# Kernel tuning notes

Measured on AMD Instinct MI355X. Metric: run time of the kernel, lower is better.

## Reference

```python
import jax, jax.numpy as jnp
import numpy as np

B, T_IN, T_OUT, D, M, N = 4, 10, 5, 5, 96, 96
H1 = 64      # hidden dim of deep ConvLSTM layers
ATTN = 32    # attention bottleneck channels
SEL = 0      # selected_dim


def _conv(x, w, b):
    # SAME conv, NCHW / OIHW
    p = (w.shape[-1] - 1) // 2
    y = jax.lax.conv_general_dilated(x, w, (1, 1), [(p, p), (p, p)],
                                     dimension_numbers=('NCHW', 'OIHW', 'NCHW'))
    return y + b[None, :, None, None]


def _cell(xt, h, c, w, b):
    # standard ConvLSTM cell (no peephole): conv over concat(x, h) -> i,f,o,g
    z = _conv(jnp.concatenate([xt, h], axis=1), w, b)
    i, f, o, g = jnp.split(z, 4, axis=1)
    c = jax.nn.sigmoid(f) * c + jax.nn.sigmoid(i) * jnp.tanh(g)
    h = jax.nn.sigmoid(o) * jnp.tanh(c)
    return h, c


def setup_inputs() -> dict:
    key = jax.random.key(0)
    ks = jax.random.split(key, 12)
    w = lambda k, s: jax.random.normal(k, s, jnp.float32) * 0.05
    z = lambda n: jnp.zeros((n,), jnp.float32)
    return {
        'x': jax.random.normal(ks[0], (B, T_IN, D, M, N), jnp.float32),
        # encoder ConvLSTM cells: hidden dims [1, H1, H1]
        'enc_w0': w(ks[1], (4 * 1, D + 1, 3, 3)), 'enc_b0': z(4 * 1),
        'enc_w1': w(ks[2], (4 * H1, 1 + H1, 3, 3)), 'enc_b1': z(4 * H1),
        'enc_w2': w(ks[3], (4 * H1, H1 + H1, 3, 3)), 'enc_b2': z(4 * H1),
        # decoder ConvLSTM cells: hidden dims [H1, H1, 1]
        'dec_w0': w(ks[4], (4 * H1, 1 + H1, 3, 3)), 'dec_b0': z(4 * H1),
        'dec_w1': w(ks[5], (4 * H1, H1 + H1, 3, 3)), 'dec_b1': z(4 * H1),
        'dec_w2': w(ks[6], (4 * 1, H1 + 1, 3, 3)), 'dec_b2': z(4 * 1),
        # input attention (DA-RNN style with convs): e_k = v(tanh(Wi*x_k + Wh*[h;c]))
        'attn_wi': w(ks[7], (ATTN, T_IN, 3, 3)), 'attn_bi': z(ATTN),
        'attn_wh': w(ks[8], (ATTN, 2, 3, 3)), 'attn_bh': z(ATTN),
        'attn_wv': w(ks[9], (1, ATTN, 3, 3)), 'attn_bv': z(1),
        # temporal_cnn: Conv2d(1 + window_in, 1, kernel_size=1) + ReLU
        'tcnn_w': w(ks[10], (1, T_IN + 1, 1, 1)), 'tcnn_b': z(1),
    }


def reference(x, enc_w0, enc_b0, enc_w1, enc_b1, enc_w2, enc_b2,
              dec_w0, dec_b0, dec_w1, dec_b1, dec_w2, dec_b2,
              attn_wi, attn_bi, attn_wh, attn_bh, attn_wv, attn_bv,
              tcnn_w, tcnn_b):
    b = x.shape[0]

    def attn_reweight(xs, h, c):
        # xs: (b, t, d, m, n); hidden term shared across the d channels
        hid_e = _conv(jnp.concatenate([h, c], axis=1), attn_wh, attn_bh)
        def per_k(xk):  # (b, t, m, n): time-as-channels
            e = jnp.tanh(_conv(xk, attn_wi, attn_bi) + hid_e)
            return _conv(e, attn_wv, attn_bv)[:, 0]  # (b, m, n)
        alpha = jax.vmap(per_k, in_axes=2, out_axes=1)(xs)  # (b, d, m, n)
        ea = jnp.exp(alpha)
        return xs * (ea / jnp.max(ea))[:, None]  # global-max normalization

    def run_layer(xs, h, c, w, bb):
        def step(carry, xt):
            hh, cc = _cell(xt, carry[0], carry[1], w, bb)
            return (hh, cc), hh
        (h, c), hs = jax.lax.scan(step, (h, c), jnp.swapaxes(xs, 0, 1))
        return jnp.swapaxes(hs, 0, 1), (h, c)

    # ---------- encoder ----------
    h0 = jnp.zeros((b, 1, M, N), x.dtype); c0 = jnp.zeros_like(h0)
    def enc0_step(carry, t):
        xs, h, c = carry
        xs = attn_reweight(xs, h, c)  # re-weight whole sequence each step
        xt = jax.lax.dynamic_index_in_dim(xs, t, axis=1, keepdims=False)
        h, c = _cell(xt, h, c, enc_w0, enc_b0)
        return (xs, h, c), h
    (_, h0, c0), hs0 = jax.lax.scan(enc0_step, (x, h0, c0), jnp.arange(T_IN))
    out0 = jnp.swapaxes(hs0, 0, 1)  # (b, T_IN, 1, m, n)

    h1 = jnp.zeros((b, H1, M, N), x.dtype); c1 = jnp.zeros_like(h1)
    out1, (h1, c1) = run_layer(out0, h1, c1, enc_w1, enc_b1)
    h2 = jnp.zeros((b, H1, M, N), x.dtype); c2 = jnp.zeros_like(h2)
    out2, (h2, c2) = run_layer(out1, h2, c2, enc_w2, enc_b2)

    # ---------- decoder (encoder states reversed) ----------
    dec_in = jnp.zeros((b, T_OUT, 1, M, N), x.dtype)
    d0, _ = run_layer(dec_in, h2, c2, dec_w0, dec_b0)
    d1, _ = run_layer(d0, h1, c1, dec_w1, dec_b1)

    y_prev = x[:, :, SEL]  # (b, T_IN, m, n): selected variable, time-as-channels
    def dec2_step(carry, xt):
        h, c, yp = carry
        h, c = _cell(xt, h, c, dec_w2, dec_b2)          # (b, 1, m, n)
        ycat = jnp.concatenate([yp, h], axis=1)         # (b, T_IN+1, m, n)
        h = jax.nn.relu(_conv(ycat, tcnn_w, tcnn_b))    # temporal 1x1 CNN readout
        return (h, c, ycat[:, 1:]), h
    _, hs = jax.lax.scan(dec2_step, (h0, c0, y_prev), jnp.swapaxes(d1, 0, 1))
    return jnp.swapaxes(hs, 0, 1)  # (b, T_OUT, 1, m, n)
```

## Files before the change

### kernel.cpp

```cpp
#include <hip/hip_runtime.h>


#define PIX  9216
#define NB   4
#define TIN  10
#define TOUT 5
#define ND   5
#define HID  64

typedef __attribute__((ext_vector_type(8))) short bf16x8;
typedef __attribute__((ext_vector_type(4))) float f32x4;

__device__ __forceinline__ float sigmf_(float x) { return 1.0f / (1.0f + __expf(-x)); }
__device__ __forceinline__ float tanhf_(float x) { return 1.0f - 2.0f / (__expf(2.0f * x) + 1.0f); }
__device__ __forceinline__ unsigned short f2bf(float f) {
    unsigned u = __float_as_uint(f);
    unsigned r = u + 0x7FFFu + ((u >> 16) & 1u);
    return (unsigned short)(r >> 16);
}
__device__ __forceinline__ float bf2f(unsigned short u) {
    return __uint_as_float(((unsigned)u) << 16);
}
__device__ __forceinline__ unsigned fmap_(float f) {
    unsigned u = __float_as_uint(f);
    return (u & 0x80000000u) ? ~u : (u | 0x80000000u);
}
__device__ __forceinline__ float funmap_(unsigned v) {
    return __uint_as_float((v & 0x80000000u) ? (v ^ 0x80000000u) : ~v);
}
__device__ __forceinline__ void gload_lds16(const void* g, void* l) {
    __builtin_amdgcn_global_load_lds(
        (const __attribute__((address_space(1))) void*)g,
        (__attribute__((address_space(3))) void*)l, 16, 0, 0);
}

template <int NCH, bool XCONV>
__device__ __forceinline__ void
cell64_body(char* smem, int bid,
            const unsigned short* __restrict__ inP,
            const unsigned short* __restrict__ wP,
            const float* __restrict__ bias,
            const float* cprev, float* cout,
            const float* __restrict__ zeropg,
            unsigned short* __restrict__ d1, int d1_coff, int d1_ncg,
            unsigned short* __restrict__ d2, int d2_coff, int d2_ncg,
            const float* __restrict__ xim, const unsigned short* __restrict__ wxP)
{
    const int lane = threadIdx.x;
    const int wv   = threadIdx.y;
    const int tid  = wv * 64 + lane;
    const int rid = (bid & 7) * 48 + (bid >> 3);
    const int y = rid % 96, b = rid / 96;
    const int l15 = lane & 15, l4 = lane >> 4;
    const int NCG = NCH * 4;

    const int scg  = tid & 3;
    const int spr0 = tid >> 2;

    auto stage = [&](char* buf, int cc) {
#pragma unroll
        for (int i = 0; i < 5; ++i) {
            int pr = spr0 + i * 64;
            int r = pr / 98;
            int p = pr - r * 98;
            int gy = y - 1 + r, gx = p - 1;
            const void* g = (const void*)zeropg;
            if (pr < 294 && (unsigned)gy < 96u && (unsigned)gx < 96u) {
                int cg = scg ^ ((p >> 1) & 3);
                g = (const void*)(inP + (((size_t)(b * NCG + cc * 4 + cg) * 9216
                                          + gy * 96 + gx) << 3));
            }
            gload_lds16(g, buf + i * 4096 + wv * 1024);
        }
    };

    f32x4 acc[4][6] = {};
    bf16x8 af[3][4];

#pragma unroll
    for (int t0 = 0; t0 < 2; ++t0)
#pragma unroll
        for (int g = 0; g < 4; ++g)
            af[t0][g] = *(const bf16x8*)(wP
                + ((size_t)(t0 * NCH + 0) * 256 + g * 64 + wv * 16 + l15) * 32 + l4 * 8);

    stage(smem, 0);
    __syncthreads();
#pragma unroll
    for (int cc = 0; cc < NCH; ++cc) {
        if (cc + 1 < NCH) stage(smem + ((cc + 1) & 1) * 20480, cc + 1);
        const char* buf = smem + (cc & 1) * 20480;
#pragma unroll
        for (int tap = 0; tap < 9; ++tap) {
            const int T = cc * 9 + tap;
            const int Tp = T + 2;
            if (Tp < NCH * 9) {
                const int cc2 = Tp / 9, tap2 = Tp % 9;
#pragma unroll
                for (int g = 0; g < 4; ++g)
                    af[Tp % 3][g] = *(const bf16x8*)(wP
                        + ((size_t)(tap2 * NCH + cc2) * 256 + g * 64 + wv * 16 + l15) * 32 + l4 * 8);
            }
            const int ky = tap / 3, kx = tap % 3;
            bf16x8 bk[6];
#pragma unroll
            for (int k = 0; k < 6; ++k) {
                int p = k * 16 + kx + l15;
                int slot = l4 ^ ((p >> 1) & 3);
                bk[k] = *(const bf16x8*)(buf + (ky * 98 + p) * 64 + slot * 16);
            }
            __builtin_amdgcn_s_setprio(1);
#pragma unroll
            for (int g = 0; g < 4; ++g)
#pragma unroll
                for (int k = 0; k < 6; ++k)
                    acc[g][k] = __builtin_amdgcn_mfma_f32_16x16x32_bf16(
                        af[T % 3][g], bk[k], acc[g][k], 0, 0, 0);
            __builtin_amdgcn_s_setprio(0);
        }
        if (cc + 1 < NCH) __syncthreads();
    }

    if (XCONV) {
        bf16x8 afx[4];
#pragma unroll
        for (int g = 0; g < 4; ++g)
            afx[g] = *(const bf16x8*)(wxP
                + ((size_t)(g * 64 + wv * 16 + l15)) * 32 + l4 * 8);
        const float* xb = xim + b * PIX;
#pragma unroll
        for (int k = 0; k < 6; ++k) {
            int p = k * 16 + l15;
            bf16x8 bx = { 0, 0, 0, 0, 0, 0, 0, 0 };
#pragma unroll
            for (int j = 0; j < 8; ++j) {
                int tap = l4 * 8 + j;
                if (tap < 9) {
                    int gy = y + tap / 3 - 1, gx = p + tap % 3 - 1;
                    if ((unsigned)gy < 96u && (unsigned)gx < 96u)
                        bx[j] = (short)f2bf(xb[gy * 96 + gx]);
                }
            }
#pragma unroll
            for (int g = 0; g < 4; ++g)
                acc[g][k] = __builtin_amdgcn_mfma_f32_16x16x32_bf16(
                    afx[g], bx, acc[g][k], 0, 0, 0);
        }
    }

#pragma unroll
    for (int r = 0; r < 4; ++r) {
        int hc = wv * 16 + l4 * 4 + r;
        float bi = bias[hc], bff = bias[64 + hc];
        float bo = bias[128 + hc], bg = bias[192 + hc];
#pragma unroll
        for (int k = 0; k < 6; ++k) {
            int px = k * 16 + l15;
            int gpix = y * 96 + px;
            float ii = sigmf_(acc[0][k][r] + bi);
            float ff = sigmf_(acc[1][k][r] + bff);
            float oo = sigmf_(acc[2][k][r] + bo);
            float gg = tanhf_(acc[3][k][r] + bg);
            int cidx = (b * HID + hc) * 9216 + gpix;
            float cn = ff * cprev[cidx] + ii * gg;
            cout[cidx] = cn;
            unsigned short hb = f2bf(oo * tanhf_(cn));
            int ch1 = d1_coff + hc;
            d1[((size_t)(b * d1_ncg + (ch1 >> 3)) * 9216 + gpix) * 8 + (ch1 & 7)] = hb;
            if (d2) {
                int ch2 = d2_coff + hc;
                d2[((size_t)(b * d2_ncg + (ch2 >> 3)) * 9216 + gpix) * 8 + (ch2 & 7)] = hb;
            }
        }
    }
}

__device__ __forceinline__ void
attnE_body(char* smem, int aid,
           const unsigned short* __restrict__ xsp, const unsigned short* __restrict__ wiP,
           const float* __restrict__ h0, const float* __restrict__ c0,
           const float* __restrict__ wh, const float* __restrict__ bh,
           const float* __restrict__ bi, unsigned short* __restrict__ eP)
{
    float* heS = (float*)smem;
    const int lane = threadIdx.x, wvid = threadIdx.y;
    const int tile = aid % 36, k = (aid / 36) % 5, bb = aid / 180;
    const int l15 = lane & 15, l4 = lane >> 4;
    const int tid = wvid * 64 + lane;

    {
        int p = tile * 256 + tid;
        int y = p / 96, x = p - y * 96;
        float hv9[9], cv9[9];
        const float* hp = h0 + bb * PIX;
        const float* cp = c0 + bb * PIX;
#pragma unroll
        for (int t9 = 0; t9 < 9; ++t9) {
            int gy = y + t9 / 3 - 1, gx = x + t9 % 3 - 1;
            bool ok = (unsigned)gy < 96u && (unsigned)gx < 96u;
            hv9[t9] = ok ? hp[gy * 96 + gx] : 0.0f;
            cv9[t9] = ok ? cp[gy * 96 + gx] : 0.0f;
        }
#pragma unroll
        for (int ch = 0; ch < 32; ++ch) {
            float a = bi[ch] + bh[ch];
#pragma unroll
            for (int t9 = 0; t9 < 9; ++t9) {
                a = fmaf(wh[(ch * 2 + 0) * 9 + t9], hv9[t9], a);
                a = fmaf(wh[(ch * 2 + 1) * 9 + t9], cv9[t9], a);
            }
            heS[tid * 33 + ch] = a;
        }
    }

    bf16x8 af[5][2];
#pragma unroll
    for (int j = 0; j < 5; ++j)
#pragma unroll
        for (int m = 0; m < 2; ++m)
            af[j][m] = *(const bf16x8*)(wiP + ((size_t)(j * 32 + m * 16 + l15)) * 32 + l4 * 8);

    const unsigned short* xb = xsp + (size_t)(bb * ND + k) * PIX * 16;
    const int p0 = tile * 256 + wvid * 64;

    f32x4 acc[4][2] = {};
#pragma unroll
    for (int nf = 0; nf < 4; ++nf) {
        int p = p0 + nf * 16 + l15;
        int y = p / 96, x = p - y * 96;
#pragma unroll
        for (int j = 0; j < 5; ++j) {
            int tp = 2 * j + (l4 >> 1);
            bf16x8 bk = { 0, 0, 0, 0, 0, 0, 0, 0 };
            if (tp < 9) {
                int gy = y + tp / 3 - 1, gx = x + tp % 3 - 1;
                if ((unsigned)gy < 96u && (unsigned)gx < 96u)
                    bk = *(const bf16x8*)(xb + ((size_t)(gy * 96 + gx)) * 16 + (l4 & 1) * 8);
            }
            acc[nf][0] = __builtin_amdgcn_mfma_f32_16x16x32_bf16(af[j][0], bk, acc[nf][0], 0, 0, 0);
            acc[nf][1] = __builtin_amdgcn_mfma_f32_16x16x32_bf16(af[j][1], bk, acc[nf][1], 0, 0, 0);
        }
    }

    __syncthreads();

#pragma unroll
    for (int nf = 0; nf < 4; ++nf) {
        int p = p0 + nf * 16 + l15;
        int pl = wvid * 64 + nf * 16 + l15;
        const float* hrow = &heS[pl * 33];
#pragma unroll
        for (int m = 0; m < 2; ++m) {
            ushort4 o;
            o.x = f2bf(tanhf_(acc[nf][m][0] + hrow[m * 16 + l4 * 4 + 0]));
            o.y = f2bf(tanhf_(acc[nf][m][1] + hrow[m * 16 + l4 * 4 + 1]));
            o.z = f2bf(tanhf_(acc[nf][m][2] + hrow[m * 16 + l4 * 4 + 2]));
            o.w = f2bf(tanhf_(acc[nf][m][3] + hrow[m * 16 + l4 * 4 + 3]));
            *(ushort4*)(eP + ((size_t)(bb * ND + k) * PIX + p) * 32 + m * 16 + l4 * 4) = o;
        }
    }
}

__device__ __forceinline__ void
alpha_body(char* smem, int aid,
           const unsigned short* __restrict__ eP, const float* __restrict__ wvv,
           const float* __restrict__ bv, float* __restrict__ alpha,
           unsigned* __restrict__ msl)
{
    const int tid = threadIdx.y * 64 + threadIdx.x;
    const int tile = aid % 36, k = (aid / 36) % 5, bb = aid / 180;
    int p = tile * 256 + tid;
    int y = p / 96, x = p - y * 96;
    const unsigned short* eb = eP + (size_t)(bb * ND + k) * PIX * 32;
    float acc = bv[0];
#pragma unroll
    for (int ky = 0; ky < 3; ++ky) {
        int gy = y + ky - 1;
        if ((unsigned)gy >= 96u) continue;
#pragma unroll
        for (int kx = 0; kx < 3; ++kx) {
            int gx = x + kx - 1;
            if ((unsigned)gx >= 96u) continue;
            int tap = ky * 3 + kx;
            const unsigned short* ee = eb + ((size_t)(gy * 96 + gx)) * 32;
#pragma unroll
            for (int cg = 0; cg < 4; ++cg) {
                bf16x8 ev = *(const bf16x8*)(ee + cg * 8);
#pragma unroll
                for (int jj = 0; jj < 8; ++jj)
                    acc = fmaf(wvv[(cg * 8 + jj) * 9 + tap], bf2f((unsigned short)ev[jj]), acc);
            }
        }
    }
    alpha[(size_t)(bb * ND + k) * PIX + p] = acc;

    float* s = (float*)smem;
    s[tid] = acc;
    __syncthreads();
    for (int st = 128; st > 0; st >>= 1) {
        if (tid < st) s[tid] = fmaxf(s[tid], s[tid + st]);
        __syncthreads();
    }
    if (tid == 0) atomicMax(msl, fmap_(s[0]));
}

__device__ __forceinline__ void
dec2_body(int did,
          const unsigned short* __restrict__ inP, int ncg, int cgbase,
          const float* __restrict__ hprev, const float* cprev,
          const unsigned short* __restrict__ wm, const float* __restrict__ w2,
          const float* __restrict__ bias,
          const float* __restrict__ tw, const float* __restrict__ tb,
          const float* __restrict__ yprev,
          float* __restrict__ ynext, float* __restrict__ hcarry,
          float* __restrict__ outp, float* cout)
{
    const int wv = threadIdx.y, lane = threadIdx.x;
    const int l15 = lane & 15, l4 = lane >> 4;
    const int bx = did % 144, b = did / 144;
    const int p0 = (bx * 4 + wv) * 16;
    const int y = p0 / 96, xbase = p0 - y * 96;
    const int x = xbase + l15;

    f32x4 acc = {0.f, 0.f, 0.f, 0.f};
#pragma unroll
    for (int ky = 0; ky < 3; ++ky) {
        int gy = y + ky - 1;
        bool oky = (unsigned)gy < 96u;
#pragma unroll
        for (int kx = 0; kx < 3; ++kx) {
            const int tap = ky * 3 + kx;
            int gx = x + kx - 1;
            bool ok = oky && ((unsigned)gx < 96u);
#pragma unroll
            for (int cc = 0; cc < 2; ++cc) {
                bf16x8 a = *(const bf16x8*)(wm + ((size_t)(tap * 2 + cc) * 16 + l15) * 32 + l4 * 8);
                bf16x8 bk = { 0, 0, 0, 0, 0, 0, 0, 0 };
                if (ok)
                    bk = *(const bf16x8*)(inP + ((size_t)(b * ncg + cgbase + cc * 4 + l4) * 9216
                                                 + gy * 96 + gx) * 8);
                acc = __builtin_amdgcn_mfma_f32_16x16x32_bf16(a, bk, acc, 0, 0, 0);
            }
        }
    }

    if (l4 == 0) {
        int px = p0 + l15;
        float aI = acc[0] + bias[0];
        float aF = acc[1] + bias[1];
        float aO = acc[2] + bias[2];
        float aG = acc[3] + bias[3];
        const float* hp = hprev + b * PIX;
#pragma unroll
        for (int ky = 0; ky < 3; ++ky) {
            int gy = y + ky - 1;
            if ((unsigned)gy >= 96u) continue;
#pragma unroll
            for (int kx = 0; kx < 3; ++kx) {
                int gx = x + kx - 1;
                if ((unsigned)gx >= 96u) continue;
                int tap = ky * 3 + kx;
                float hv = hp[gy * 96 + gx];
                aI = fmaf(w2[(0 * 65 + 64) * 9 + tap], hv, aI);
                aF = fmaf(w2[(1 * 65 + 64) * 9 + tap], hv, aF);
                aO = fmaf(w2[(2 * 65 + 64) * 9 + tap], hv, aO);
                aG = fmaf(w2[(3 * 65 + 64) * 9 + tap], hv, aG);
            }
        }
        int idx = b * PIX + px;
        float cn = sigmf_(aF) * cprev[idx] + sigmf_(aI) * tanhf_(aG);
        cout[idx] = cn;
        float h = sigmf_(aO) * tanhf_(cn);

        float a2 = tb[0];
#pragma unroll
        for (int c2 = 0; c2 < TIN; ++c2)
            a2 = fmaf(tw[c2], yprev[(size_t)(b * TIN + c2) * PIX + px], a2);
        a2 = fmaf(tw[TIN], h, a2);
        float o = fmaxf(a2, 0.0f);
        outp[(size_t)b * TOUT * PIX + px] = o;
#pragma unroll
        for (int c2 = 0; c2 < TIN - 1; ++c2)
            ynext[(size_t)(b * TIN + c2) * PIX + px] = yprev[(size_t)(b * TIN + c2 + 1) * PIX + px];
        ynext[(size_t)(b * TIN + 9) * PIX + px] = h;
        hcarry[idx] = o;
    }
}

template <int NCH, bool XCONV, bool ATTN>
__global__ void __launch_bounds__(256, 2)
mk_cell_attnE(const unsigned short* __restrict__ inP, const unsigned short* __restrict__ wP,
              const float* __restrict__ bias, const float* cprev, float* cout,
              const float* __restrict__ zeropg,
              unsigned short* __restrict__ d1, int d1_coff, int d1_ncg,
              unsigned short* __restrict__ d2, int d2_coff, int d2_ncg,
              const float* __restrict__ xim, const unsigned short* __restrict__ wxP,
              const unsigned short* __restrict__ xsp, const unsigned short* __restrict__ wiP,
              const float* __restrict__ h0, const float* __restrict__ c0,
              const float* __restrict__ wh, const float* __restrict__ bh,
              const float* __restrict__ bi, unsigned short* __restrict__ eP)
{
    __shared__ __align__(16) char smem[40960];
    if (blockIdx.x < 384)
        cell64_body<NCH, XCONV>(smem, blockIdx.x, inP, wP, bias, cprev, cout, zeropg,
                                d1, d1_coff, d1_ncg, d2, d2_coff, d2_ncg, xim, wxP);
    else if (ATTN)
        attnE_body(smem, blockIdx.x - 384, xsp, wiP, h0, c0, wh, bh, bi, eP);
}

template <int NCH, bool ATTN>
__global__ void __launch_bounds__(256, 2)
mk_cell_alpha(const unsigned short* __restrict__ inP, const unsigned short* __restrict__ wP,
              const float* __restrict__ bias, const float* cprev, float* cout,
              const float* __restrict__ zeropg,
              unsigned short* __restrict__ d1, int d1_coff, int d1_ncg,
              unsigned short* __restrict__ d2, int d2_coff, int d2_ncg,
              const unsigned short* __restrict__ eP, const float* __restrict__ wvv,
              const float* __restrict__ bv, float* __restrict__ alpha,
              unsigned* __restrict__ msl)
{
    __shared__ __align__(16) char smem[40960];
    if (blockIdx.x < 384)
        cell64_body<NCH, false>(smem, blockIdx.x, inP, wP, bias, cprev, cout, zeropg,
                                d1, d1_coff, d1_ncg, d2, d2_coff, d2_ncg, nullptr, nullptr);
    else if (ATTN)
        alpha_body(smem, blockIdx.x - 384, eP, wvv, bv, alpha, msl);
}

__global__ void __launch_bounds__(256)
mk_scale_small5(const float* __restrict__ xs_cur, float* __restrict__ xs_nxt,
                unsigned short* __restrict__ xsp,
                const float* __restrict__ alpha, const unsigned* __restrict__ msl,
                int ts,
                const float* __restrict__ h0in, const float* cprev,
                const float* __restrict__ w, const float* __restrict__ bias,
                float* __restrict__ h0out, float* cout)
{
    __shared__ float z[4][64];
    const int bid = blockIdx.x;
    const float mval = funmap_(msl[0]);
    if (bid < 720) {
        int idx = bid * 256 + threadIdx.x;
        int p = idx % PIX;
        int q = idx / PIX;
        int d = q % ND, bb = q / ND;
        float wgt = __expf(alpha[idx] - mval);
        unsigned short tmp[16];
#pragma unroll
        for (int t = 0; t < TIN; ++t) {
            size_t xi = ((size_t)(bb * TIN + t) * ND + d) * PIX + p;
            float v = xs_cur[xi] * wgt;
            xs_nxt[xi] = v;
            tmp[t] = f2bf(v);
        }
#pragma unroll
        for (int t = TIN; t < 16; ++t) tmp[t] = 0;
        uint4* dst = (uint4*)(xsp + (size_t)idx * 16);
        dst[0] = *(uint4*)&tmp[0];
        dst[1] = *(uint4*)&tmp[8];
    } else {
        int bid2 = bid - 720;
        int bx = bid2 % 144, bb = bid2 / 144;
        const int pxl = threadIdx.x & 63, gate = threadIdx.x >> 6;
        const int p = bx * 64 + pxl;
        const int y = p / 96, x = p - y * 96;
        float acc = bias[gate];
#pragma unroll
        for (int cin = 0; cin < 6; ++cin) {
            const float* wp = w + (gate * 6 + cin) * 9;
#pragma unroll
            for (int ky = 0; ky < 3; ++ky) {
                int gy = y + ky - 1;
                if ((unsigned)gy >= 96u) continue;
#pragma unroll
                for (int kx = 0; kx < 3; ++kx) {
                    int gx = x + kx - 1;
                    if ((unsigned)gx >= 96u) continue;
                    int np = gy * 96 + gx;
                    float v;
                    if (cin < 5) {
                        float raw = xs_cur[((size_t)(bb * TIN + ts) * ND + cin) * PIX + np];
                        v = raw * __expf(alpha[(size_t)(bb * ND + cin) * PIX + np] - mval);
                    } else {
                        v = h0in[bb * PIX + np];
                    }
                    acc = fmaf(wp[ky * 3 + kx], v, acc);
                }
            }
        }
        z[gate][pxl] = acc;
        __syncthreads();
        if (threadIdx.x < 64) {
            int pp = bx * 64 + threadIdx.x;
            int idx = bb * PIX + pp;
            float cn = sigmf_(z[1][threadIdx.x]) * cprev[idx]
                     + sigmf_(z[0][threadIdx.x]) * tanhf_(z[3][threadIdx.x]);
            cout[idx] = cn;
            h0out[idx] = sigmf_(z[2][threadIdx.x]) * tanhf_(cn);
        }
    }
}

template <bool HAS0, bool HAS2>
__global__ void __launch_bounds__(256, 2)
mk_dec(const unsigned short* __restrict__ d1in, const unsigned short* __restrict__ wpd1,
       const float* __restrict__ b1, float* c1, unsigned short* __restrict__ d1out,
       const float* __restrict__ zeropg,
       const unsigned short* __restrict__ d0in, const unsigned short* __restrict__ wpd0,
       const float* __restrict__ b0, float* c2, unsigned short* __restrict__ d0out,
       unsigned short* __restrict__ d1next,
       const unsigned short* __restrict__ d2in,
       const float* __restrict__ hprev, float* c0,
       const unsigned short* __restrict__ wd2m, const float* __restrict__ w2,
       const float* __restrict__ b2,
       const float* __restrict__ tw, const float* __restrict__ tb,
       const float* __restrict__ yprev, float* __restrict__ ynext,
       float* __restrict__ hcarry, float* __restrict__ outp)
{
    __shared__ __align__(16) char smem[40960];
    if (blockIdx.x < 384) {
        cell64_body<4, false>(smem, blockIdx.x, d1in, wpd1, b1, c1, c1, zeropg,
                              d1out, 64, 16, nullptr, 0, 0, nullptr, nullptr);
    } else if (blockIdx.x < 768) {
        if (HAS0)
            cell64_body<2, false>(smem, blockIdx.x - 384, d0in, wpd0, b0, c2, c2, zeropg,
                                  d0out, 0, 8, d1next, 0, 16, nullptr, nullptr);
    } else {
        if (HAS2)
            dec2_body(blockIdx.x - 768, d2in, 16, 8, hprev, c0, wd2m, w2, b2,
                      tw, tb, yprev, ynext, hcarry, outp, c0);
    }
}

template <int NCH>
__global__ void __launch_bounds__(256, 2)
cell_k(const unsigned short* __restrict__ inP, const unsigned short* __restrict__ wP,
       const float* __restrict__ bias, const float* cprev, float* cout,
       const float* __restrict__ zeropg,
       unsigned short* __restrict__ d1, int d1_coff, int d1_ncg,
       unsigned short* __restrict__ d2, int d2_coff, int d2_ncg)
{
    __shared__ __align__(16) char smem[40960];
    cell64_body<NCH, false>(smem, blockIdx.x, inP, wP, bias, cprev, cout, zeropg,
                            d1, d1_coff, d1_ncg, d2, d2_coff, d2_ncg, nullptr, nullptr);
}

__global__ void __launch_bounds__(256)
dec2_k(const unsigned short* __restrict__ d2in, const float* __restrict__ hprev,
       float* c0, const unsigned short* __restrict__ wd2m, const float* __restrict__ w2,
       const float* __restrict__ b2, const float* __restrict__ tw, const float* __restrict__ tb,
       const float* __restrict__ yprev, float* __restrict__ ynext,
       float* __restrict__ hcarry, float* __restrict__ outp)
{
    dec2_body(blockIdx.x, d2in, 16, 8, hprev, c0, wd2m, w2, b2,
              tw, tb, yprev, ynext, hcarry, outp, c0);
}

__global__ void __launch_bounds__(256)
attn_e_k(const unsigned short* __restrict__ xsp, const unsigned short* __restrict__ wiP,
         const float* __restrict__ h0, const float* __restrict__ c0,
         const float* __restrict__ wh, const float* __restrict__ bh,
         const float* __restrict__ bi, unsigned short* __restrict__ eP)
{
    __shared__ __align__(16) char smem[33792];
    attnE_body(smem, blockIdx.x, xsp, wiP, h0, c0, wh, bh, bi, eP);
}

__global__ void __launch_bounds__(256)
alpha_k(const unsigned short* __restrict__ eP, const float* __restrict__ wvv,
        const float* __restrict__ bv, float* __restrict__ alpha, unsigned* __restrict__ msl)
{
    __shared__ __align__(16) char smem[1024];
    alpha_body(smem, blockIdx.x, eP, wvv, bv, alpha, msl);
}

__global__ void __launch_bounds__(256)
prep_kernel(const float* __restrict__ enc_w1, const float* __restrict__ enc_w2,
            const float* __restrict__ dec_w0, const float* __restrict__ dec_w1,
            const float* __restrict__ dec_w2, const float* __restrict__ attn_wi,
            const float* __restrict__ x,
            unsigned short* __restrict__ wpe1, unsigned short* __restrict__ wpe2,
            unsigned short* __restrict__ wpd0, unsigned short* __restrict__ wpd1,
            unsigned short* __restrict__ wd2m, unsigned short* __restrict__ wiP,
            unsigned short* __restrict__ wxP,
            unsigned short* __restrict__ xsp, float* __restrict__ yp)
{
    int gid = blockIdx.x;
    auto wpack = [&](const float* w, unsigned short* wp, int WCIN, int NCH,
                     int coff, int climit, int base) {
        int idx = (gid - base) * 256 + threadIdx.x;
        if (idx >= 9 * NCH * 256 * 32) return;
        int k = idx & 31;
        int ocp = (idx >> 5) & 255;
        int rest = idx >> 13;
        int cc = rest % NCH, tap = rest / NCH;
        int hc = ocp >> 2, gate = ocp & 3;
        int c = cc * 32 + k;
        float v = 0.0f;
        if (c < climit) v = w[((gate * 64 + hc) * WCIN + (c + coff)) * 9 + tap];
        wp[idx] = f2bf(v);
    };
    if (gid < 576) { wpack(enc_w1, wpe1, 65, 2, 1, 64, 0); return; }
    if (gid < 1728) { wpack(enc_w2, wpe2, 128, 4, 0, 128, 576); return; }
    if (gid < 2304) { wpack(dec_w0, wpd0, 65, 2, 1, 64, 1728); return; }
    if (gid < 3456) { wpack(dec_w1, wpd1, 128, 4, 0, 128, 2304); return; }
    if (gid < 3492) {
        int idx = (gid - 3456) * 256 + threadIdx.x;
        if (idx < 9 * 2 * 16 * 32) {
            int k = idx & 31;
            int oc = (idx >> 5) & 15;
            int cc = (idx >> 9) & 1;
            int tap = idx >> 10;
            float v = 0.0f;
            if (oc < 4) v = dec_w2[(oc * 65 + cc * 32 + k) * 9 + tap];
            wd2m[idx] = f2bf(v);
        }
        return;
    }
    if (gid < 3512) {
        int idx = (gid - 3492) * 256 + threadIdx.x;
        if (idx < 5120) {
            int kl = idx & 31, oc = (idx >> 5) & 31, j = idx >> 10;
            int tappos = kl >> 4, ch = kl & 15;
            int tap = 2 * j + tappos;
            float v = 0.0f;
            if (tap < 9 && ch < 10) v = attn_wi[(oc * TIN + ch) * 9 + tap];
            wiP[idx] = f2bf(v);
        }
        return;
    }
    if (gid < 3544) {
        int idx = (gid - 3512) * 256 + threadIdx.x;
        if (idx < 8192) {
            int s = idx & 31;
            int ocp = idx >> 5;
            int hc = ocp >> 2, gate = ocp & 3;
            float v = 0.0f;
            if (s < 9) v = enc_w1[((gate * 64 + hc) * 65 + 0) * 9 + s];
            wxP[idx] = f2bf(v);
        }
        return;
    }
    if (gid < 4264) {
        int idx = (gid - 3544) * 256 + threadIdx.x;
        int p = idx % PIX;
        int q = idx / PIX;
        int d = q % ND, bb = q / ND;
        unsigned short tmp[16];
#pragma unroll
        for (int t = 0; t < TIN; ++t)
            tmp[t] = f2bf(x[((size_t)(bb * TIN + t) * ND + d) * PIX + p]);
#pragma unroll
        for (int t = TIN; t < 16; ++t) tmp[t] = 0;
        uint4* dst = (uint4*)(xsp + (size_t)idx * 16);
        dst[0] = *(uint4*)&tmp[0];
        dst[1] = *(uint4*)&tmp[8];
        return;
    }
    {
        int idx = (gid - 4264) * 256 + threadIdx.x;
        int p = idx % PIX;
        int q = idx / PIX;
        yp[idx] = x[(size_t)(q * ND + 0) * PIX + p];
    }
}

extern "C" void kernel_launch(void* const* d_in, const int* in_sizes, int n_in,
                              void* d_out, int out_size, void* d_ws, size_t ws_size,
                              hipStream_t stream)
{
    const float* x       = (const float*)d_in[0];
    const float* enc_w0  = (const float*)d_in[1];
    const float* enc_b0  = (const float*)d_in[2];
    const float* enc_w1  = (const float*)d_in[3];
    const float* enc_b1  = (const float*)d_in[4];
    const float* enc_w2  = (const float*)d_in[5];
    const float* enc_b2  = (const float*)d_in[6];
    const float* dec_w0  = (const float*)d_in[7];
    const float* dec_b0  = (const float*)d_in[8];
    const float* dec_w1  = (const float*)d_in[9];
    const float* dec_b1  = (const float*)d_in[10];
    const float* dec_w2  = (const float*)d_in[11];
    const float* dec_b2  = (const float*)d_in[12];
    const float* attn_wi = (const float*)d_in[13];
    const float* attn_bi = (const float*)d_in[14];
    const float* attn_wh = (const float*)d_in[15];
    const float* attn_bh = (const float*)d_in[16];
    const float* attn_wv = (const float*)d_in[17];
    const float* attn_bv = (const float*)d_in[18];
    const float* tcnn_w  = (const float*)d_in[19];
    const float* tcnn_b  = (const float*)d_in[20];
    float* out = (float*)d_out;

    char* cur = (char*)d_ws;
    auto alloc = [&](size_t bytes) { char* p = cur; cur += (bytes + 255) & ~(size_t)255; return p; };
    float* xsA  = (float*)alloc((size_t)NB * TIN * ND * PIX * 4);
    float* xsB  = (float*)alloc((size_t)NB * TIN * ND * PIX * 4);
    float* alp  = (float*)alloc((size_t)NB * ND * PIX * 4);
    float* ypa  = (float*)alloc((size_t)NB * TIN * PIX * 4);
    float* ypb  = (float*)alloc((size_t)NB * TIN * PIX * 4);
    unsigned short* wpe1 = (unsigned short*)alloc((size_t)9 * 2 * 256 * 32 * 2);
    unsigned short* wpe2 = (unsigned short*)alloc((size_t)9 * 4 * 256 * 32 * 2);
    unsigned short* wpd0 = (unsigned short*)alloc((size_t)9 * 2 * 256 * 32 * 2);
    unsigned short* wpd1 = (unsigned short*)alloc((size_t)9 * 4 * 256 * 32 * 2);
    unsigned short* wd2m = (unsigned short*)alloc((size_t)9 * 2 * 16 * 32 * 2);
    unsigned short* wiP  = (unsigned short*)alloc(5120 * 2);
    unsigned short* wxP  = (unsigned short*)alloc(8192 * 2);
    unsigned short* xsp  = (unsigned short*)alloc((size_t)NB * ND * PIX * 16 * 2);
    unsigned short* eP   = (unsigned short*)alloc((size_t)NB * ND * PIX * 32 * 2);
    char* zbeg = cur;
    float* h0a  = (float*)alloc(NB * PIX * 4);
    float* h0b  = (float*)alloc(NB * PIX * 4);
    float* c0   = (float*)alloc(NB * PIX * 4);
    float* c1   = (float*)alloc((size_t)NB * HID * PIX * 4);
    float* c2   = (float*)alloc((size_t)NB * HID * PIX * 4);
    const size_t IN1_B = (size_t)NB * 8 * PIX * 8 * 2;
    const size_t IN2_B = (size_t)NB * 16 * PIX * 8 * 2;
    unsigned short* In1a = (unsigned short*)alloc(IN1_B);
    unsigned short* In1b = (unsigned short*)alloc(IN1_B);
    unsigned short* In2a = (unsigned short*)alloc(IN2_B);
    unsigned short* In2b = (unsigned short*)alloc(IN2_B);
    unsigned* mslot = (unsigned*)alloc(256);
    float* zeropg = (float*)alloc(256);
    char* zend = cur;

    hipMemcpyAsync(xsA, x, (size_t)NB * TIN * ND * PIX * 4, hipMemcpyDeviceToDevice, stream);
    hipMemsetAsync(zbeg, 0, (size_t)(zend - zbeg), stream);
    prep_kernel<<<dim3(5704), 256, 0, stream>>>(enc_w1, enc_w2, dec_w0, dec_w1, dec_w2,
                                                attn_wi, x, wpe1, wpe2, wpd0, wpd1,
                                                wd2m, wiP, wxP, xsp, ypa);

    dim3 blk(64, 4);
    float *h0 = h0a, *h0n = h0b;
    float *xc = xsA, *xn = xsB;
    unsigned short *i1c = In1a, *i1n = In1b, *i2c = In2a, *i2n = In2b;

    attn_e_k<<<dim3(720), blk, 0, stream>>>(xsp, wiP, h0, c0, attn_wh, attn_bh, attn_bi, eP);
    alpha_k<<<dim3(720), blk, 0, stream>>>(eP, attn_wv, attn_bv, alp, mslot + 0);
    mk_scale_small5<<<dim3(1296), 256, 0, stream>>>(xc, xn, xsp, alp, mslot + 0, 0,
                                                    h0, c0, enc_w0, enc_b0, h0n, c0);
    { float* tmp = h0; h0 = h0n; h0n = tmp; }
    { float* tmp = xc; xc = xn; xn = tmp; }

    for (int t = 0; t < TIN; ++t) {
        const bool hn = (t < TIN - 1);
        unsigned short* e1d1 = hn ? i1n : In2a;
        int e1o = hn ? 0 : 64;
        int e1n = hn ? 8 : 16;
        unsigned short* e2d1 = hn ? i2n : In1a;
        int e2o = hn ? 64 : 0;
        int e2n = hn ? 16 : 8;
        int grid = 384 + (hn ? 720 : 0);

        if (hn)
            mk_cell_attnE<2, true, true><<<dim3(grid), blk, 0, stream>>>(
                i1c, wpe1, enc_b1, c1, c1, zeropg, e1d1, e1o, e1n, i2c, 0, 16,
                h0, wxP,
                xsp, wiP, h0, c0, attn_wh, attn_bh, attn_bi, eP);
        else
            mk_cell_attnE<2, true, false><<<dim3(grid), blk, 0, stream>>>(
                i1c, wpe1, enc_b1, c1, c1, zeropg, e1d1, e1o, e1n, i2c, 0, 16,
                h0, wxP,
                xsp, wiP, h0, c0, attn_wh, attn_bh, attn_bi, eP);

        if (hn)
            mk_cell_alpha<4, true><<<dim3(grid), blk, 0, stream>>>(
                i2c, wpe2, enc_b2, c2, c2, zeropg, e2d1, e2o, e2n, nullptr, 0, 0,
                eP, attn_wv, attn_bv, alp, mslot + t + 1);
        else
            mk_cell_alpha<4, false><<<dim3(grid), blk, 0, stream>>>(
                i2c, wpe2, enc_b2, c2, c2, zeropg, e2d1, e2o, e2n, nullptr, 0, 0,
                eP, attn_wv, attn_bv, alp, mslot + t + 1);

        if (hn) {
            mk_scale_small5<<<dim3(1296), 256, 0, stream>>>(xc, xn, xsp, alp, mslot + t + 1,
                                                            t + 1, h0, c0, enc_w0, enc_b0,
                                                            h0n, c0);
            { float* tmp = h0; h0 = h0n; h0n = tmp; }
            { float* tmp = xc; xc = xn; xn = tmp; }
        }
        { unsigned short* tmp = i1c; i1c = i1n; i1n = tmp; }
        { unsigned short* tmp = i2c; i2c = i2n; i2n = tmp; }
    }

    float *hc = h0, *hcn = h0n;
    cell_k<2><<<dim3(384), blk, 0, stream>>>(In1a, wpd0, dec_b0, c2, c2, zeropg,
                                             In1b, 0, 8, In2a, 0, 16);
    mk_dec<true, false><<<dim3(768), blk, 0, stream>>>(
        In2a, wpd1, dec_b1, c1, In2b, zeropg,
        In1b, wpd0, dec_b0, c2, In1a, In2b,
        nullptr, nullptr, nullptr, nullptr, nullptr, nullptr, nullptr, nullptr,
        nullptr, nullptr, nullptr, nullptr);
    mk_dec<true, true><<<dim3(1344), blk, 0, stream>>>(
        In2b, wpd1, dec_b1, c1, In2a, zeropg,
        In1a, wpd0, dec_b0, c2, In1b, In2a,
        In2b, hc, c0, wd2m, dec_w2, dec_b2, tcnn_w, tcnn_b,
        ypa, ypb, hcn, out + 0 * PIX);
    mk_dec<true, true><<<dim3(1344), blk, 0, stream>>>(
        In2a, wpd1, dec_b1, c1, In2b, zeropg,
        In1b, wpd0, dec_b0, c2, In1a, In2b,
        In2a, hcn, c0, wd2m, dec_w2, dec_b2, tcnn_w, tcnn_b,
        ypb, ypa, hc, out + 1 * PIX);
    mk_dec<true, true><<<dim3(1344), blk, 0, stream>>>(
        In2b, wpd1, dec_b1, c1, In2a, zeropg,
        In1a, wpd0, dec_b0, c2, In1b, In2a,
        In2b, hc, c0, wd2m, dec_w2, dec_b2, tcnn_w, tcnn_b,
        ypa, ypb, hcn, out + 2 * PIX);
    mk_dec<false, true><<<dim3(1344), blk, 0, stream>>>(
        In2a, wpd1, dec_b1, c1, In2b, zeropg,
        nullptr, nullptr, nullptr, nullptr, nullptr, nullptr,
        In2a, hcn, c0, wd2m, dec_w2, dec_b2, tcnn_w, tcnn_b,
        ypb, ypa, hc, out + 3 * PIX);
    dec2_k<<<dim3(576), blk, 0, stream>>>(In2b, hc, c0, wd2m, dec_w2, dec_b2,
                                          tcnn_w, tcnn_b, ypa, ypb, hcn, out + 4 * PIX);
}
```

Baseline: 1.280 ms.

## Wavefront-pipeline encoder layers so layer-2 step t runs with layer-1 step t+1

Restructures the encoder schedule as a diagonal wavefront. A new fused kernel runs the layer-2 cell for one timestep, the layer-1 cell for the next timestep and the attention-energy blocks in one launch, with a prologue and epilogue around the loop. The alpha computation moves out of the fused cell kernel into its own launch. The aim is fewer serialized launches per timestep and more concurrent blocks filling the GPU, at the cost of trickier buffer ping-pong indexing that must be exactly right.

```diff
diff --git a/kernel.cpp b/kernel.cpp
--- a/kernel.cpp
+++ b/kernel.cpp
@@ -387,7 +387,30 @@
     }
 }
 
-template <int NCH, bool XCONV, bool ATTN>
+__global__ void __launch_bounds__(256, 2)
+mk_enc(const unsigned short* __restrict__ i2in, const unsigned short* __restrict__ wpe2,
+       const float* __restrict__ b2, float* c2, unsigned short* __restrict__ i2n_hi,
+       const float* __restrict__ zeropg,
+       const unsigned short* __restrict__ i1in, const unsigned short* __restrict__ wpe1,
+       const float* __restrict__ b1, float* c1,
+       unsigned short* __restrict__ i1out, unsigned short* __restrict__ i2n_lo,
+       const float* __restrict__ xim, const unsigned short* __restrict__ wxP,
+       const unsigned short* __restrict__ xsp, const unsigned short* __restrict__ wiP,
+       const float* __restrict__ h0, const float* __restrict__ c0,
+       const float* __restrict__ wh, const float* __restrict__ bh,
+       const float* __restrict__ bi, unsigned short* __restrict__ eP)
+{
+    __shared__ __align__(16) char smem[40960];
+    if (blockIdx.x < 384)
+        cell64_body<4, false>(smem, blockIdx.x, i2in, wpe2, b2, c2, c2, zeropg,
+                              i2n_hi, 64, 16, nullptr, 0, 0, nullptr, nullptr);
+    else if (blockIdx.x < 768)
+        cell64_body<2, true>(smem, blockIdx.x - 384, i1in, wpe1, b1, c1, c1, zeropg,
+                             i1out, 0, 8, i2n_lo, 0, 16, xim, wxP);
+    else
+        attnE_body(smem, blockIdx.x - 768, xsp, wiP, h0, c0, wh, bh, bi, eP);
+}
+
 __global__ void __launch_bounds__(256, 2)
 mk_cell_attnE(const unsigned short* __restrict__ inP, const unsigned short* __restrict__ wP,
               const float* __restrict__ bias, const float* cprev, float* cout,
@@ -402,29 +425,10 @@
 {
     __shared__ __align__(16) char smem[40960];
     if (blockIdx.x < 384)
-        cell64_body<NCH, XCONV>(smem, blockIdx.x, inP, wP, bias, cprev, cout, zeropg,
-                                d1, d1_coff, d1_ncg, d2, d2_coff, d2_ncg, xim, wxP);
-    else if (ATTN)
+        cell64_body<2, true>(smem, blockIdx.x, inP, wP, bias, cprev, cout, zeropg,
+                             d1, d1_coff, d1_ncg, d2, d2_coff, d2_ncg, xim, wxP);
+    else
         attnE_body(smem, blockIdx.x - 384, xsp, wiP, h0, c0, wh, bh, bi, eP);
-}
-
-template <int NCH, bool ATTN>
-__global__ void __launch_bounds__(256, 2)
-mk_cell_alpha(const unsigned short* __restrict__ inP, const unsigned short* __restrict__ wP,
-              const float* __restrict__ bias, const float* cprev, float* cout,
-              const float* __restrict__ zeropg,
-              unsigned short* __restrict__ d1, int d1_coff, int d1_ncg,
-              unsigned short* __restrict__ d2, int d2_coff, int d2_ncg,
-              const unsigned short* __restrict__ eP, const float* __restrict__ wvv,
-              const float* __restrict__ bv, float* __restrict__ alpha,
-              unsigned* __restrict__ msl)
-{
-    __shared__ __align__(16) char smem[40960];
-    if (blockIdx.x < 384)
-        cell64_body<NCH, false>(smem, blockIdx.x, inP, wP, bias, cprev, cout, zeropg,
-                                d1, d1_coff, d1_ncg, d2, d2_coff, d2_ncg, nullptr, nullptr);
-    else if (ATTN)
-        alpha_body(smem, blockIdx.x - 384, eP, wvv, bv, alpha, msl);
 }
 
 __global__ void __launch_bounds__(256)
@@ -532,17 +536,18 @@
     }
 }
 
-template <int NCH>
+template <int NCH, bool XCONV>
 __global__ void __launch_bounds__(256, 2)
 cell_k(const unsigned short* __restrict__ inP, const unsigned short* __restrict__ wP,
        const float* __restrict__ bias, const float* cprev, float* cout,
        const float* __restrict__ zeropg,
        unsigned short* __restrict__ d1, int d1_coff, int d1_ncg,
-       unsigned short* __restrict__ d2, int d2_coff, int d2_ncg)
+       unsigned short* __restrict__ d2, int d2_coff, int d2_ncg,
+       const float* __restrict__ xim, const unsigned short* __restrict__ wxP)
 {
     __shared__ __align__(16) char smem[40960];
-    cell64_body<NCH, false>(smem, blockIdx.x, inP, wP, bias, cprev, cout, zeropg,
-                            d1, d1_coff, d1_ncg, d2, d2_coff, d2_ncg, nullptr, nullptr);
+    cell64_body<NCH, XCONV>(smem, blockIdx.x, inP, wP, bias, cprev, cout, zeropg,
+                            d1, d1_coff, d1_ncg, d2, d2_coff, d2_ncg, xim, wxP);
 }
 
 __global__ void __launch_bounds__(256)
@@ -733,7 +738,8 @@
     dim3 blk(64, 4);
     float *h0 = h0a, *h0n = h0b;
     float *xc = xsA, *xn = xsB;
-    unsigned short *i1c = In1a, *i1n = In1b, *i2c = In2a, *i2n = In2b;
+    unsigned short* In1[2] = { In1a, In1b };
+    unsigned short* In2[2] = { In2a, In2b };
 
     attn_e_k<<<dim3(720), blk, 0, stream>>>(xsp, wiP, h0, c0, attn_wh, attn_bh, attn_bi, eP);
     alpha_k<<<dim3(720), blk, 0, stream>>>(eP, attn_wv, attn_bv, alp, mslot + 0);
@@ -741,51 +747,49 @@
                                                     h0, c0, enc_w0, enc_b0, h0n, c0);
     { float* tmp = h0; h0 = h0n; h0n = tmp; }
     { float* tmp = xc; xc = xn; xn = tmp; }
-
-    for (int t = 0; t < TIN; ++t) {
-        const bool hn = (t < TIN - 1);
-        unsigned short* e1d1 = hn ? i1n : In2a;
-        int e1o = hn ? 0 : 64;
-        int e1n = hn ? 8 : 16;
-        unsigned short* e2d1 = hn ? i2n : In1a;
-        int e2o = hn ? 64 : 0;
-        int e2n = hn ? 16 : 8;
-        int grid = 384 + (hn ? 720 : 0);
-
-        if (hn)
-            mk_cell_attnE<2, true, true><<<dim3(grid), blk, 0, stream>>>(
-                i1c, wpe1, enc_b1, c1, c1, zeropg, e1d1, e1o, e1n, i2c, 0, 16,
-                h0, wxP,
-                xsp, wiP, h0, c0, attn_wh, attn_bh, attn_bi, eP);
-        else
-            mk_cell_attnE<2, true, false><<<dim3(grid), blk, 0, stream>>>(
-                i1c, wpe1, enc_b1, c1, c1, zeropg, e1d1, e1o, e1n, i2c, 0, 16,
-                h0, wxP,
-                xsp, wiP, h0, c0, attn_wh, attn_bh, attn_bi, eP);
-
-        if (hn)
-            mk_cell_alpha<4, true><<<dim3(grid), blk, 0, stream>>>(
-                i2c, wpe2, enc_b2, c2, c2, zeropg, e2d1, e2o, e2n, nullptr, 0, 0,
-                eP, attn_wv, attn_bv, alp, mslot + t + 1);
-        else
-            mk_cell_alpha<4, false><<<dim3(grid), blk, 0, stream>>>(
-                i2c, wpe2, enc_b2, c2, c2, zeropg, e2d1, e2o, e2n, nullptr, 0, 0,
-                eP, attn_wv, attn_bv, alp, mslot + t + 1);
-
-        if (hn) {
-            mk_scale_small5<<<dim3(1296), 256, 0, stream>>>(xc, xn, xsp, alp, mslot + t + 1,
-                                                            t + 1, h0, c0, enc_w0, enc_b0,
-                                                            h0n, c0);
-            { float* tmp = h0; h0 = h0n; h0n = tmp; }
-            { float* tmp = xc; xc = xn; xn = tmp; }
-        }
-        { unsigned short* tmp = i1c; i1c = i1n; i1n = tmp; }
-        { unsigned short* tmp = i2c; i2c = i2n; i2n = tmp; }
-    }
+    mk_cell_attnE<<<dim3(1104), blk, 0, stream>>>(In1[0], wpe1, enc_b1, c1, c1, zeropg,
+                                                  In1[1], 0, 8, In2[0], 0, 16,
+                                                  h0, wxP,
+                                                  xsp, wiP, h0, c0,
+                                                  attn_wh, attn_bh, attn_bi, eP);
+    alpha_k<<<dim3(720), blk, 0, stream>>>(eP, attn_wv, attn_bv, alp, mslot + 1);
+    mk_scale_small5<<<dim3(1296), 256, 0, stream>>>(xc, xn, xsp, alp, mslot + 1, 1,
+                                                    h0, c0, enc_w0, enc_b0, h0n, c0);
+    { float* tmp = h0; h0 = h0n; h0n = tmp; }
+    { float* tmp = xc; xc = xn; xn = tmp; }
+
+    for (int k = 0; k <= 7; ++k) {
+        unsigned short* i2k = In2[k & 1];
+        unsigned short* i2n = In2[(k + 1) & 1];
+        unsigned short* i1in  = In1[(k + 1) & 1];
+        unsigned short* i1out = In1[k & 1];
+        mk_enc<<<dim3(1488), blk, 0, stream>>>(
+            i2k, wpe2, enc_b2, c2, i2n, zeropg,
+            i1in, wpe1, enc_b1, c1, i1out, i2n,
+            h0, wxP,
+            xsp, wiP, h0, c0, attn_wh, attn_bh, attn_bi, eP);
+        alpha_k<<<dim3(720), blk, 0, stream>>>(eP, attn_wv, attn_bv, alp, mslot + k + 2);
+        mk_scale_small5<<<dim3(1296), 256, 0, stream>>>(xc, xn, xsp, alp, mslot + k + 2,
+                                                        k + 2, h0, c0, enc_w0, enc_b0,
+                                                        h0n, c0);
+        { float* tmp = h0; h0 = h0n; h0n = tmp; }
+        { float* tmp = xc; xc = xn; xn = tmp; }
+    }
+
+    cell_k<4, false><<<dim3(384), blk, 0, stream>>>(In2[0], wpe2, enc_b2, c2, c2, zeropg,
+                                                    In2[1], 64, 16, nullptr, 0, 0,
+                                                    nullptr, nullptr);
+    cell_k<2, true><<<dim3(384), blk, 0, stream>>>(In1[1], wpe1, enc_b1, c1, c1, zeropg,
+                                                   In2a, 64, 16, In2[1], 0, 16,
+                                                   h0, wxP);
+    cell_k<4, false><<<dim3(384), blk, 0, stream>>>(In2[1], wpe2, enc_b2, c2, c2, zeropg,
+                                                    In1a, 0, 8, nullptr, 0, 0,
+                                                    nullptr, nullptr);
 
     float *hc = h0, *hcn = h0n;
-    cell_k<2><<<dim3(384), blk, 0, stream>>>(In1a, wpd0, dec_b0, c2, c2, zeropg,
-                                             In1b, 0, 8, In2a, 0, 16);
+    cell_k<2, false><<<dim3(384), blk, 0, stream>>>(In1a, wpd0, dec_b0, c2, c2, zeropg,
+                                                    In1b, 0, 8, In2a, 0, 16,
+                                                    nullptr, nullptr);
     mk_dec<true, false><<<dim3(768), blk, 0, stream>>>(
         In2a, wpd1, dec_b1, c1, In2b, zeropg,
         In1b, wpd0, dec_b0, c2, In1a, In2b,
```

Measured after the change: 1.313 ms. 2.5% more time.
